# Optimization experiments

Measured on AMD Instinct MI355X. Metric: run time of the kernel, lower is better.

Reference implementation:

```python
import jax, jax.numpy as jnp
import numpy as np

BN_EPS = 1e-5

def _conv1x1(x, W, b):
    # x: [B,C,H,W], W: [O,C], b: [O]
    return jnp.einsum('bchw,oc->bohw', x, W) + b[None, :, None, None]

def setup_inputs() -> dict:
    key = jax.random.key(0)
    ks = jax.random.split(key, 9)
    B, C, H, W = 8, 256, 64, 64
    Ci = C // 2
    s_in = 0.05  # small init scale to keep softmax well-conditioned
    return {
        'x': jax.random.normal(ks[0], (B, C, H, W), jnp.float32),
        'theta_w': jax.random.normal(ks[1], (Ci, C), jnp.float32) * s_in,
        'theta_b': jnp.zeros((Ci,), jnp.float32),
        'phi_w': jax.random.normal(ks[2], (Ci, C), jnp.float32) * s_in,
        'phi_b': jnp.zeros((Ci,), jnp.float32),
        'g_w': jax.random.normal(ks[3], (Ci, C), jnp.float32) * s_in,
        'g_b': jnp.zeros((Ci,), jnp.float32),
        'out_w': jax.random.normal(ks[4], (C, Ci), jnp.float32) * s_in,
        'out_b': jnp.zeros((C,), jnp.float32),
        'gamma': jnp.ones((C,), jnp.float32),
        'beta': jnp.zeros((C,), jnp.float32),
    }

def reference(x, theta_w, theta_b, phi_w, phi_b, g_w, g_b, out_w, out_b, gamma, beta):
    B, C, H, W = x.shape
    Ci = C // 2
    N = H * W
    theta = _conv1x1(x, theta_w, theta_b).reshape(B, Ci, N)  # [B,Ci,N]
    phi = _conv1x1(x, phi_w, phi_b).reshape(B, Ci, N)        # [B,Ci,N]
    g = _conv1x1(x, g_w, g_b).reshape(B, Ci, N)              # [B,Ci,N]
    scale = 1.0 / jnp.sqrt(jnp.asarray(Ci, x.dtype))
    sim = jnp.einsum('bcn,bcm->bnm', theta, phi) * scale     # [B,N,N]
    attn = jax.nn.softmax(sim, axis=-1)
    y = jnp.einsum('bnm,bcm->bcn', attn, g).reshape(B, Ci, H, W)
    y = _conv1x1(y, out_w, out_b)                            # [B,C,H,W]
    # BatchNorm2d, training-mode statistics (biased variance), as in torch default
    mean = y.mean(axis=(0, 2, 3))
    var = y.var(axis=(0, 2, 3))
    y = (y - mean[None, :, None, None]) * jax.lax.rsqrt(var + BN_EPS)[None, :, None, None]
    y = y * gamma[None, :, None, None] + beta[None, :, None, None]
    return x + y
```

## Files before the change

kernel.cpp:

```cpp
#include <hip/hip_runtime.h>
#include <hip/hip_bf16.h>

typedef __bf16 bf16x8 __attribute__((ext_vector_type(8)));
typedef float f32x4 __attribute__((ext_vector_type(4)));
typedef float f32x16 __attribute__((ext_vector_type(16)));

#define B_ 8
#define C_ 256
#define CI 128
#define N_ 4096

__device__ __forceinline__ float exp2fast(float x) {
    return __builtin_amdgcn_exp2f(x);
}
__device__ __forceinline__ ushort f2bf(float f) {
    union { float f; unsigned u; } v; v.f = f;
    unsigned r = v.u + 0x7fffu + ((v.u >> 16) & 1u);
    return (ushort)(r >> 16);
}
__device__ __forceinline__ float bf2f(ushort u) {
    union { unsigned u; float f; } v; v.u = ((unsigned)u) << 16;
    return v.f;
}
__device__ __forceinline__ unsigned cvtpk(float lo, float hi) {
    unsigned r;
    asm("v_cvt_pk_bf16_f32 %0, %1, %2" : "=v"(r) : "v"(lo), "v"(hi));
    return r;
}
__device__ __forceinline__ void plswap(unsigned& a, unsigned& b) {
    asm volatile("v_permlane32_swap_b32 %0, %1" : "+v"(a), "+v"(b));
}
__device__ __forceinline__ void gld16(const void* src, void* dst) {
    __builtin_amdgcn_global_load_lds(
        (const __attribute__((address_space(1))) unsigned*)src,
        (__attribute__((address_space(3))) unsigned*)dst, 16, 0, 0);
}

__global__ void k_prep(const float* __restrict__ tw, const float* __restrict__ pw,
                       const float* __restrict__ gw, const float* __restrict__ ow,
                       ushort* __restrict__ wbf, ushort* __restrict__ owbf) {
    int idx = blockIdx.x * 256 + threadIdx.x;
    if (idx < 384 * 256) {
        int i = idx >> 8, c = idx & 255;
        float v = (i < 128) ? tw[i * 256 + c]
                : (i < 256) ? pw[(i - 128) * 256 + c]
                            : gw[(i - 256) * 256 + c];
        wbf[idx] = f2bf(v);
    }
    if (idx < 256 * 128) owbf[idx] = f2bf(ow[idx]);
}

__global__ __launch_bounds__(256) void k_transpose(const float* __restrict__ x,
                                                   ushort* __restrict__ xt) {
    __shared__ __align__(16) float tile[64][65];
    int b = blockIdx.z, c0 = blockIdx.y * 64, n0 = blockIdx.x * 64;
    int t = threadIdx.x;
    int cl = t >> 2, nc = (t & 3) * 16;
    const float* src = x + ((size_t)(b * 256 + c0 + cl)) * N_ + n0 + nc;
#pragma unroll
    for (int j = 0; j < 4; j++) {
        float4 v = *reinterpret_cast<const float4*>(src + 4 * j);
        tile[cl][nc + 4 * j + 0] = v.x;
        tile[cl][nc + 4 * j + 1] = v.y;
        tile[cl][nc + 4 * j + 2] = v.z;
        tile[cl][nc + 4 * j + 3] = v.w;
    }
    __syncthreads();
    int nl = t >> 2, cc = (t & 3) * 16;
    ushort* dst = xt + ((size_t)b * N_ + n0 + nl) * 256 + c0 + cc;
#pragma unroll
    for (int j = 0; j < 4; j++) {
        ushort4 o;
        o.x = f2bf(tile[cc + 4 * j + 0][nl]);
        o.y = f2bf(tile[cc + 4 * j + 1][nl]);
        o.z = f2bf(tile[cc + 4 * j + 2][nl]);
        o.w = f2bf(tile[cc + 4 * j + 3][nl]);
        *reinterpret_cast<ushort4*>(dst + 4 * j) = o;
    }
}

__global__ __launch_bounds__(256) void k_qkv(const ushort* __restrict__ wbf,
                                             const ushort* __restrict__ xt,
                                             const float* __restrict__ tb,
                                             const float* __restrict__ pb,
                                             const float* __restrict__ gb,
                                             ushort* __restrict__ qt,
                                             ushort* __restrict__ kt,
                                             ushort* __restrict__ gv) {
    __shared__ __align__(16) ushort lt[4][64][72];
    int nt = blockIdx.x, it = blockIdx.y, b = blockIdx.z;
    int tid = threadIdx.x, w = tid >> 6, l = tid & 63, lr = l & 15, lg = l >> 4;
    int i_off = it * 128 + (w >> 1) * 64;
    int n_off = nt * 128 + (w & 1) * 64;
    const ushort* xb = xt + (size_t)b * N_ * 256;

    f32x4 acc[4][4];
#pragma unroll
    for (int i = 0; i < 4; i++)
#pragma unroll
        for (int j = 0; j < 4; j++) acc[i][j] = (f32x4)0.0f;

#pragma unroll
    for (int kc = 0; kc < 8; kc++) {
        int ko = kc * 32 + lg * 8;
        bf16x8 a[4], bb[4];
#pragma unroll
        for (int fi = 0; fi < 4; fi++)
            a[fi] = *reinterpret_cast<const bf16x8*>(wbf + (size_t)(i_off + fi * 16 + lr) * 256 + ko);
#pragma unroll
        for (int fn = 0; fn < 4; fn++)
            bb[fn] = *reinterpret_cast<const bf16x8*>(xb + (size_t)(n_off + fn * 16 + lr) * 256 + ko);
#pragma unroll
        for (int fi = 0; fi < 4; fi++)
#pragma unroll
            for (int fn = 0; fn < 4; fn++)
                acc[fi][fn] = __builtin_amdgcn_mfma_f32_16x16x32_bf16(a[fi], bb[fn], acc[fi][fn], 0, 0, 0);
    }

    const float* bias = (it == 0) ? tb : (it == 1) ? pb : gb;
    const float mul = (it == 0) ? (0.08838834764831845f * 1.4426950408889634f) : 1.0f;
    if (it == 2) {
        ushort* g = gv + (size_t)b * CI * N_;
#pragma unroll
        for (int fi = 0; fi < 4; fi++)
#pragma unroll
            for (int reg = 0; reg < 4; reg++) {
                int cl = (w >> 1) * 64 + fi * 16 + lg * 4 + reg;
                float bv = bias[cl];
#pragma unroll
                for (int fn = 0; fn < 4; fn++)
                    g[(size_t)cl * N_ + n_off + fn * 16 + lr] = f2bf(acc[fi][fn][reg] + bv);
            }
    } else {
#pragma unroll
        for (int fi = 0; fi < 4; fi++)
#pragma unroll
            for (int reg = 0; reg < 4; reg++) {
                int il = fi * 16 + lg * 4 + reg;
                float bv = bias[(w >> 1) * 64 + il];
#pragma unroll
                for (int fn = 0; fn < 4; fn++)
                    lt[w][fn * 16 + lr][il] = f2bf((acc[fi][fn][reg] + bv) * mul);
            }
        __builtin_amdgcn_s_waitcnt(0);
        ushort* dst = ((it == 0) ? qt : kt) + (size_t)b * N_ * CI;
        ushort* drow = dst + (size_t)(n_off + l) * CI + (w >> 1) * 64;
#pragma unroll
        for (int cc = 0; cc < 8; cc++) {
            uint4 v = *reinterpret_cast<uint4*>(&lt[w][l][cc * 8]);
            *reinterpret_cast<uint4*>(drow + cc * 8) = v;
        }
    }
}

__global__ __launch_bounds__(256, 2) void k_attn(const ushort* __restrict__ qt,
                                                 const ushort* __restrict__ kt,
                                                 const ushort* __restrict__ gv,
                                                 ushort* __restrict__ yt) {
    __shared__ __align__(16) char smem[65536];
    int bid = blockIdx.x;
    int b = bid & 7, qb = bid >> 3;
    int tid = threadIdx.x, w = tid >> 6, l = tid & 63;
    int p = w >> 1, s = w & 1;
    int l31 = l & 31, lh = l >> 5;
    const ushort* qtb = qt + (size_t)b * N_ * CI;
    const ushort* ktb = kt + (size_t)b * N_ * CI;
    const ushort* gvb = gv + (size_t)b * CI * N_;
    char* kbuf = smem + p * 16384;
    char* vbuf = smem + 32768 + p * 16384;
    const int pbase = p * 2048;
    const int nq = qb * 64 + s * 32;
    const int q = nq + l31;
    const int swk = (l31 & 7) << 4;
    const int swv = (l31 & 3) << 4;

    bf16x8 qf[8];
#pragma unroll
    for (int kc = 0; kc < 8; kc++)
        qf[kc] = *reinterpret_cast<const bf16x8*>(qtb + (size_t)q * CI + kc * 16 + lh * 8);

    f32x16 acc[4];
#pragma unroll
    for (int fc = 0; fc < 4; fc++) acc[fc] = (f32x16)0.0f;
    float lrun = 0.f;

#define STAGE(t_, bi)                                                              \
    do {                                                                           \
        int m0_ = pbase + (t_) * 32;                                               \
        const char* ks_ = (const char*)(ktb + (size_t)m0_ * CI);                   \
        const char* vs_ = (const char*)(gvb + (size_t)m0_);                        \
        char* kd_ = kbuf + (bi) * 8192;                                            \
        char* vd_ = vbuf + (bi) * 8192;                                            \
        _Pragma("unroll")                                                          \
        for (int i_ = 0; i_ < 4; ++i_) {                                           \
            int cc = i_ * 128 + s * 64 + l;                                        \
            int m_ = cc >> 4, hb = (cc & 15) << 4;                                 \
            gld16(ks_ + m_ * 256 + (hb ^ ((m_ & 7) << 4)), kd_ + cc * 16);         \
        }                                                                          \
        _Pragma("unroll")                                                          \
        for (int i_ = 0; i_ < 4; ++i_) {                                           \
            int cc = i_ * 128 + s * 64 + l;                                        \
            int c_ = cc >> 2, hb = (cc & 3) << 4;                                  \
            gld16(vs_ + (size_t)c_ * (N_ * 2) + (hb ^ ((c_ & 3) << 4)),            \
                  vd_ + cc * 16);                                                  \
        }                                                                          \
    } while (0)

    STAGE(0, 0);
    __syncthreads();

    for (int t = 0; t < 64; ++t) {
        int cur = t & 1;
        if (t < 63) STAGE(t + 1, cur ^ 1);
        const char* kbc = kbuf + cur * 8192;
        const char* vbc = vbuf + cur * 8192;

        f32x16 S = (f32x16)0.0f;
        __builtin_amdgcn_s_setprio(1);
#pragma unroll
        for (int kc = 0; kc < 8; kc++) {
            bf16x8 kf = *reinterpret_cast<const bf16x8*>(
                kbc + l31 * 256 + ((kc * 32 + lh * 16) ^ swk));
            S = __builtin_amdgcn_mfma_f32_32x32x16_bf16(kf, qf[kc], S, 0, 0, 0);
        }
        __builtin_amdgcn_s_setprio(0);

        float pv[16];
        float rs = 0.f;
#pragma unroll
        for (int r = 0; r < 16; r++) {
            pv[r] = exp2fast(S[r]);
            rs += pv[r];
        }
        rs += __shfl_xor(rs, 32);
        lrun += rs;

        unsigned u0 = cvtpk(pv[0], pv[1]),  u1 = cvtpk(pv[2], pv[3]);
        unsigned u2 = cvtpk(pv[4], pv[5]),  u3 = cvtpk(pv[6], pv[7]);
        unsigned u4 = cvtpk(pv[8], pv[9]),  u5 = cvtpk(pv[10], pv[11]);
        unsigned u6 = cvtpk(pv[12], pv[13]), u7 = cvtpk(pv[14], pv[15]);
        plswap(u0, u2);
        plswap(u1, u3);
        plswap(u4, u6);
        plswap(u5, u7);
        union { unsigned u[4]; bf16x8 v; } pb0, pb1;
        pb0.u[0] = u0; pb0.u[1] = u1; pb0.u[2] = u2; pb0.u[3] = u3;
        pb1.u[0] = u4; pb1.u[1] = u5; pb1.u[2] = u6; pb1.u[3] = u7;

        __builtin_amdgcn_s_setprio(1);
#pragma unroll
        for (int mk = 0; mk < 2; mk++) {
            bf16x8 pf = mk ? pb1.v : pb0.v;
#pragma unroll
            for (int fc = 0; fc < 4; fc++) {
                bf16x8 vf = *reinterpret_cast<const bf16x8*>(
                    vbc + (fc * 32 + l31) * 64 + ((mk * 32 + lh * 16) ^ swv));
                acc[fc] = __builtin_amdgcn_mfma_f32_32x32x16_bf16(vf, pf, acc[fc], 0, 0, 0);
            }
        }
        __builtin_amdgcn_s_setprio(0);
        __syncthreads();
    }
#undef STAGE

    float* accb = (float*)smem;
    float* mlb = (float*)(smem + 34816);
    if (p == 0) {
        float* ab = accb + s * (64 * 68) + l * 68;
#pragma unroll
        for (int fc = 0; fc < 4; fc++)
            *reinterpret_cast<f32x16*>(ab + fc * 16) = acc[fc];
        if (l < 32) mlb[s * 32 + l] = lrun;
    }
    __syncthreads();
    if (p == 1) {
        float l0 = mlb[s * 32 + l31];
        float inv = 1.f / (lrun + l0);
        const float* ab = accb + s * (64 * 68) + l * 68;
        ushort* yb = yt + (size_t)b * N_ * CI + (size_t)q * CI;
#pragma unroll
        for (int fc = 0; fc < 4; fc++) {
            f32x16 a0 = *reinterpret_cast<const f32x16*>(ab + fc * 16);
#pragma unroll
            for (int rg = 0; rg < 4; rg++) {
                ushort4 o;
                o.x = f2bf((acc[fc][rg * 4 + 0] + a0[rg * 4 + 0]) * inv);
                o.y = f2bf((acc[fc][rg * 4 + 1] + a0[rg * 4 + 1]) * inv);
                o.z = f2bf((acc[fc][rg * 4 + 2] + a0[rg * 4 + 2]) * inv);
                o.w = f2bf((acc[fc][rg * 4 + 3] + a0[rg * 4 + 3]) * inv);
                *reinterpret_cast<ushort4*>(yb + fc * 32 + rg * 8 + lh * 4) = o;
            }
        }
    }
}

__global__ __launch_bounds__(256) void k_outconv(const ushort* __restrict__ owbf,
                                                 const ushort* __restrict__ yt,
                                                 const float* __restrict__ ob,
                                                 ushort* __restrict__ pre,
                                                 float* __restrict__ part) {
    int nt = blockIdx.x, ot = blockIdx.y, b = blockIdx.z;
    int tid = threadIdx.x, w = tid >> 6, l = tid & 63, lr = l & 15, lg = l >> 4;
    int o_off = ot * 128 + (w >> 1) * 64;
    int n_off = nt * 128 + (w & 1) * 64;
    const ushort* yb = yt + (size_t)b * N_ * CI;

    f32x4 acc[4][4];
#pragma unroll
    for (int i = 0; i < 4; i++)
#pragma unroll
        for (int j = 0; j < 4; j++) acc[i][j] = (f32x4)0.0f;

#pragma unroll
    for (int kc = 0; kc < 4; kc++) {
        int ko = kc * 32 + lg * 8;
        bf16x8 a[4], bb[4];
#pragma unroll
        for (int fo = 0; fo < 4; fo++)
            a[fo] = *reinterpret_cast<const bf16x8*>(owbf + (size_t)(o_off + fo * 16 + lr) * CI + ko);
#pragma unroll
        for (int fn = 0; fn < 4; fn++)
            bb[fn] = *reinterpret_cast<const bf16x8*>(yb + (size_t)(n_off + fn * 16 + lr) * CI + ko);
#pragma unroll
        for (int fo = 0; fo < 4; fo++)
#pragma unroll
            for (int fn = 0; fn < 4; fn++)
                acc[fo][fn] = __builtin_amdgcn_mfma_f32_16x16x32_bf16(a[fo], bb[fn], acc[fo][fn], 0, 0, 0);
    }

    ushort* pb_ = pre + (size_t)b * C_ * N_;
#pragma unroll
    for (int fo = 0; fo < 4; fo++)
#pragma unroll
        for (int reg = 0; reg < 4; reg++) {
            int o = o_off + fo * 16 + lg * 4 + reg;
            float bv = ob[o];
            float s1 = 0.f, s2 = 0.f;
#pragma unroll
            for (int fn = 0; fn < 4; fn++) {
                float v = acc[fo][fn][reg] + bv;
                pb_[(size_t)o * N_ + n_off + fn * 16 + lr] = f2bf(v);
                s1 += v;
                s2 += v * v;
            }
#pragma unroll
            for (int d = 1; d < 16; d <<= 1) {
                s1 += __shfl_xor(s1, d);
                s2 += __shfl_xor(s2, d);
            }
            if (lr == 0) {
                int slot = (b * 32 + nt) * 2 + (w & 1);
                part[((size_t)o * 512 + slot) * 2 + 0] = s1;
                part[((size_t)o * 512 + slot) * 2 + 1] = s2;
            }
        }
}

__global__ void k_stats(const float* __restrict__ part, const float* __restrict__ gamma,
                        const float* __restrict__ beta, float* __restrict__ stats) {
    int o = blockIdx.x, t = threadIdx.x;
    __shared__ float r1[256], r2[256];
    float s1 = part[((size_t)o * 512 + t) * 2 + 0] + part[((size_t)o * 512 + t + 256) * 2 + 0];
    float s2 = part[((size_t)o * 512 + t) * 2 + 1] + part[((size_t)o * 512 + t + 256) * 2 + 1];
    r1[t] = s1; r2[t] = s2;
    __syncthreads();
    for (int s = 128; s > 0; s >>= 1) {
        if (t < s) { r1[t] += r1[t + s]; r2[t] += r2[t + s]; }
        __syncthreads();
    }
    if (t == 0) {
        float cnt = 1.f / (float)(B_ * N_);
        float mean = r1[0] * cnt;
        float var = r2[0] * cnt - mean * mean;
        float inv = rsqrtf(var + 1e-5f);
        float a = gamma[o] * inv;
        stats[o * 2 + 0] = a;
        stats[o * 2 + 1] = beta[o] - mean * a;
    }
}

__global__ void k_final(const float* __restrict__ x, const ushort* __restrict__ pre,
                        const float* __restrict__ stats, float* __restrict__ out) {
    int idx = blockIdx.x * 256 + threadIdx.x;
    int o = (idx >> 10) & 255;
    float a = stats[o * 2 + 0], c = stats[o * 2 + 1];
    float4 xv = reinterpret_cast<const float4*>(x)[idx];
    ushort4 pv = reinterpret_cast<const ushort4*>(pre)[idx];
    float4 ov;
    ov.x = xv.x + bf2f(pv.x) * a + c;
    ov.y = xv.y + bf2f(pv.y) * a + c;
    ov.z = xv.z + bf2f(pv.z) * a + c;
    ov.w = xv.w + bf2f(pv.w) * a + c;
    reinterpret_cast<float4*>(out)[idx] = ov;
}

extern "C" void kernel_launch(void* const* d_in, const int* in_sizes, int n_in,
                              void* d_out, int out_size, void* d_ws, size_t ws_size,
                              hipStream_t stream) {
    const float* x  = (const float*)d_in[0];
    const float* tw = (const float*)d_in[1];
    const float* tb = (const float*)d_in[2];
    const float* pw = (const float*)d_in[3];
    const float* pb = (const float*)d_in[4];
    const float* gw = (const float*)d_in[5];
    const float* gb = (const float*)d_in[6];
    const float* ow = (const float*)d_in[7];
    const float* ob = (const float*)d_in[8];
    const float* gamma = (const float*)d_in[9];
    const float* beta  = (const float*)d_in[10];

    char* ws = (char*)d_ws;
    const size_t WBF_OFF  = 0;
    const size_t OWBF_OFF = WBF_OFF + 196608;
    const size_t XT_OFF   = OWBF_OFF + 65536;
    const size_t QT_OFF   = XT_OFF + 16777216;
    const size_t KT_OFF   = QT_OFF + 8388608;
    const size_t GV_OFF   = KT_OFF + 8388608;
    const size_t YT_OFF   = GV_OFF + 8388608;
    const size_t PRE_OFF  = YT_OFF + 8388608;
    const size_t PART_OFF = PRE_OFF + 16777216;
    const size_t ST_OFF   = PART_OFF + 1048576;

    ushort* wbf  = (ushort*)(ws + WBF_OFF);
    ushort* owbf = (ushort*)(ws + OWBF_OFF);
    ushort* xt   = (ushort*)(ws + XT_OFF);
    ushort* qt   = (ushort*)(ws + QT_OFF);
    ushort* kt   = (ushort*)(ws + KT_OFF);
    ushort* gv   = (ushort*)(ws + GV_OFF);
    ushort* yt   = (ushort*)(ws + YT_OFF);
    ushort* pre  = (ushort*)(ws + PRE_OFF);
    float*  part = (float*)(ws + PART_OFF);
    float*  stats= (float*)(ws + ST_OFF);

    k_prep<<<384, 256, 0, stream>>>(tw, pw, gw, ow, wbf, owbf);
    k_transpose<<<dim3(64, 4, 8), 256, 0, stream>>>(x, xt);
    k_qkv<<<dim3(32, 3, 8), 256, 0, stream>>>(wbf, xt, tb, pb, gb, qt, kt, gv);
    k_attn<<<512, 256, 0, stream>>>(qt, kt, gv, yt);
    k_outconv<<<dim3(32, 2, 8), 256, 0, stream>>>(owbf, yt, ob, pre, part);
    k_stats<<<256, 256, 0, stream>>>(part, gamma, beta, stats);
    k_final<<<8192, 256, 0, stream>>>(x, pre, stats, (float*)d_out);
}
```

Before: 170.1 us.

## Store g in attention-tile blocked layout and split QK accumulation chains

The g projection is now written in a pre-blocked layout matching the attention kernel's LDS tile, with 32-column groups made contiguous and channels interleaved. Each V tile stage becomes one contiguous 8 KB copy instead of strided row loads, and the LDS read uses a precomputed swizzled offset. The QK^T MFMA chain is split into two independent accumulators to shorten the dependency chain. The per-tile row-sum shuffle is moved out of the loop to a single shuffle at the end. The risks are scattered 2-byte stores in the projection kernel and extra registers for the second accumulator.

Result: no change. 168.2 us, median of 3 (-1.1%).

```diff
diff --git a/kernel.cpp b/kernel.cpp
--- a/kernel.cpp
+++ b/kernel.cpp
@@ -120,16 +120,21 @@
     const float* bias = (it == 0) ? tb : (it == 1) ? pb : gb;
     const float mul = (it == 0) ? (0.08838834764831845f * 1.4426950408889634f) : 1.0f;
     if (it == 2) {
-        ushort* g = gv + (size_t)b * CI * N_;
+        char* g = (char*)(gv + (size_t)b * CI * N_);
 #pragma unroll
         for (int fi = 0; fi < 4; fi++)
 #pragma unroll
             for (int reg = 0; reg < 4; reg++) {
                 int cl = (w >> 1) * 64 + fi * 16 + lg * 4 + reg;
                 float bv = bias[cl];
-#pragma unroll
-                for (int fn = 0; fn < 4; fn++)
-                    g[(size_t)cl * N_ + n_off + fn * 16 + lr] = f2bf(acc[fi][fn][reg] + bv);
+                int cbyte = (cl & 7) * 16 + (cl >> 3) * 512;
+#pragma unroll
+                for (int fn = 0; fn < 4; fn++) {
+                    int n = n_off + fn * 16 + lr;
+                    size_t byte = (size_t)(n >> 5) * 8192 + cbyte
+                                + ((n >> 3) & 3) * 128 + (n & 7) * 2;
+                    *(ushort*)(g + byte) = f2bf(acc[fi][fn][reg] + bv);
+                }
             }
     } else {
 #pragma unroll
@@ -172,7 +177,7 @@
     const int nq = qb * 64 + s * 32;
     const int q = nq + l31;
     const int swk = (l31 & 7) << 4;
-    const int swv = (l31 & 3) << 4;
+    const int vrb = (l31 & 7) * 16 + lh * 128 + (l31 >> 3) * 512;
 
     bf16x8 qf[8];
 #pragma unroll
@@ -188,7 +193,7 @@
     do {                                                                           \
         int m0_ = pbase + (t_) * 32;                                               \
         const char* ks_ = (const char*)(ktb + (size_t)m0_ * CI);                   \
-        const char* vs_ = (const char*)(gvb + (size_t)m0_);                        \
+        const char* vs_ = (const char*)gvb + (size_t)m0_ * 256;                    \
         char* kd_ = kbuf + (bi) * 8192;                                            \
         char* vd_ = vbuf + (bi) * 8192;                                            \
         _Pragma("unroll")                                                          \
@@ -200,9 +205,7 @@
         _Pragma("unroll")                                                          \
         for (int i_ = 0; i_ < 4; ++i_) {                                           \
             int cc = i_ * 128 + s * 64 + l;                                        \
-            int c_ = cc >> 2, hb = (cc & 3) << 4;                                  \
-            gld16(vs_ + (size_t)c_ * (N_ * 2) + (hb ^ ((c_ & 3) << 4)),            \
-                  vd_ + cc * 16);                                                  \
+            gld16(vs_ + cc * 16, vd_ + cc * 16);                                   \
         }                                                                          \
     } while (0)
 
@@ -215,13 +218,16 @@
         const char* kbc = kbuf + cur * 8192;
         const char* vbc = vbuf + cur * 8192;
 
-        f32x16 S = (f32x16)0.0f;
+        f32x16 Sa = (f32x16)0.0f, Sb = (f32x16)0.0f;
         __builtin_amdgcn_s_setprio(1);
 #pragma unroll
-        for (int kc = 0; kc < 8; kc++) {
-            bf16x8 kf = *reinterpret_cast<const bf16x8*>(
+        for (int kc = 0; kc < 8; kc += 2) {
+            bf16x8 kf0 = *reinterpret_cast<const bf16x8*>(
                 kbc + l31 * 256 + ((kc * 32 + lh * 16) ^ swk));
-            S = __builtin_amdgcn_mfma_f32_32x32x16_bf16(kf, qf[kc], S, 0, 0, 0);
+            bf16x8 kf1 = *reinterpret_cast<const bf16x8*>(
+                kbc + l31 * 256 + (((kc + 1) * 32 + lh * 16) ^ swk));
+            Sa = __builtin_amdgcn_mfma_f32_32x32x16_bf16(kf0, qf[kc], Sa, 0, 0, 0);
+            Sb = __builtin_amdgcn_mfma_f32_32x32x16_bf16(kf1, qf[kc + 1], Sb, 0, 0, 0);
         }
         __builtin_amdgcn_s_setprio(0);
 
@@ -229,10 +235,9 @@
         float rs = 0.f;
 #pragma unroll
         for (int r = 0; r < 16; r++) {
-            pv[r] = exp2fast(S[r]);
+            pv[r] = exp2fast(Sa[r] + Sb[r]);
             rs += pv[r];
         }
-        rs += __shfl_xor(rs, 32);
         lrun += rs;
 
         unsigned u0 = cvtpk(pv[0], pv[1]),  u1 = cvtpk(pv[2], pv[3]);
@@ -253,8 +258,7 @@
             bf16x8 pf = mk ? pb1.v : pb0.v;
 #pragma unroll
             for (int fc = 0; fc < 4; fc++) {
-                bf16x8 vf = *reinterpret_cast<const bf16x8*>(
-                    vbc + (fc * 32 + l31) * 64 + ((mk * 32 + lh * 16) ^ swv));
+                bf16x8 vf = *reinterpret_cast<const bf16x8*>(vbc + vrb + mk * 256 + fc * 2048);
                 acc[fc] = __builtin_amdgcn_mfma_f32_32x32x16_bf16(vf, pf, acc[fc], 0, 0, 0);
             }
         }
@@ -262,6 +266,8 @@
         __syncthreads();
     }
 #undef STAGE
+
+    lrun += __shfl_xor(lrun, 32);
 
     float* accb = (float*)smem;
     float* mlb = (float*)(smem + 34816);
```
